# Kernel tuning notes

Measured on AMD Instinct MI355X. Metric: run time of the kernel, lower is better.

The kernel has to match this reference:

```python
import jax, jax.numpy as jnp
import numpy as np

B, S, E, H, FF = 8, 1024, 1024, 16, 4096
DK = E // H
EPS = 1.1920929e-07  # torch RMSNorm default eps = finfo(float32).eps


def _rmsnorm(x, g):
    return x * jax.lax.rsqrt(jnp.mean(x * x, axis=-1, keepdims=True) + EPS) * g


def _rope(q, k):
    # q, k: [B, H, S, DK]; standard rotate-half RoPE, theta=10000
    d = q.shape[-1]
    s = q.shape[-2]
    inv_freq = 1.0 / (10000.0 ** (jnp.arange(0, d, 2, dtype=jnp.float32) / d))
    ang = jnp.arange(s, dtype=jnp.float32)[:, None] * inv_freq  # [S, d/2]
    cos = jnp.concatenate([jnp.cos(ang), jnp.cos(ang)], axis=-1)  # [S, d]
    sin = jnp.concatenate([jnp.sin(ang), jnp.sin(ang)], axis=-1)

    def rot(x):
        x1, x2 = jnp.split(x, 2, axis=-1)
        return jnp.concatenate([-x2, x1], axis=-1)

    return q * cos + rot(q) * sin, k * cos + rot(k) * sin


def setup_inputs() -> dict:
    key = jax.random.key(0)
    ks = jax.random.split(key, 16)
    sc = 0.02
    inp = {
        "x": jax.random.normal(ks[0], (B, S, E), dtype=jnp.float32),
        "WQ": jax.random.normal(ks[1], (E, E), dtype=jnp.float32) * sc,
        "bQ": jnp.zeros((E,), jnp.float32),
        "WK": jax.random.normal(ks[2], (E, E), dtype=jnp.float32) * sc,
        "bK": jnp.zeros((E,), jnp.float32),
        "WV": jax.random.normal(ks[3], (E, E), dtype=jnp.float32) * sc,
        "bV": jnp.zeros((E,), jnp.float32),
        "WO": jax.random.normal(ks[4], (E, E), dtype=jnp.float32) * sc,
        "bO": jnp.zeros((E,), jnp.float32),
        "W1": jax.random.normal(ks[5], (E, FF), dtype=jnp.float32) * sc,
        "b1": jnp.zeros((FF,), jnp.float32),
        "W2": jax.random.normal(ks[6], (FF, E), dtype=jnp.float32) * sc,
        "b2": jnp.zeros((E,), jnp.float32),
        "g1": jnp.ones((E,), jnp.float32),
        "g2": jnp.ones((E,), jnp.float32),
    }
    return inp


def reference(x, WQ, bQ, WK, bK, WV, bV, WO, bO, W1, b1, W2, b2, g1, g2):
    b, s, e = x.shape

    def attn(h):
        q = (h @ WQ + bQ).reshape(b, s, H, DK).transpose(0, 2, 1, 3)
        k = (h @ WK + bK).reshape(b, s, H, DK).transpose(0, 2, 1, 3)
        v = (h @ WV + bV).reshape(b, s, H, DK).transpose(0, 2, 1, 3)
        q, k = _rope(q, k)
        scores = jnp.einsum("bhqd,bhkd->bhqk", q, k) / jnp.sqrt(jnp.float32(DK))
        p = jax.nn.softmax(scores, axis=-1)
        o = jnp.einsum("bhqk,bhkd->bhqd", p, v)
        o = o.transpose(0, 2, 1, 3).reshape(b, s, e)
        return o @ WO + bO

    def ffn(h):
        return jax.nn.relu(h @ W1 + b1) @ W2 + b2

    x = x + attn(_rmsnorm(x, g1))
    x = x + ffn(_rmsnorm(x, g2))
    return x
```

## Files before the change

kernel.cpp:

```cpp
#include <hip/hip_runtime.h>
#include <math.h>

#define B_ 8
#define S_ 1024
#define E_ 1024
#define H_ 16
#define FF_ 4096

typedef __attribute__((ext_vector_type(8))) short bf16x8;
typedef __attribute__((ext_vector_type(4))) float f32x4;

#define QSCALE 0.1803368801111f
#define LG2_10K 0.4152410118f

__device__ __forceinline__ unsigned short f2bf(float f) {
  union { float f; unsigned u; } v;
  v.f = f;
  unsigned r = v.u + 0x7fffu + ((v.u >> 16) & 1u);
  return (unsigned short)(r >> 16);
}
__device__ __forceinline__ float bf2f(unsigned short u) {
  union { unsigned u; float f; } v;
  v.u = ((unsigned)u) << 16;
  return v.f;
}
__device__ __forceinline__ unsigned fbits(float f) {
  union { float f; unsigned u; } v;
  v.f = f;
  return v.u;
}

__device__ __forceinline__ void glds16(const void* g, void* l) {
  __builtin_amdgcn_global_load_lds(
      (const __attribute__((address_space(1))) unsigned int*)g,
      (__attribute__((address_space(3))) unsigned int*)l, 16, 0, 0);
}

__global__ __launch_bounds__(256) void prep(const float* __restrict__ WQ,
                                            const float* __restrict__ WK,
                                            const float* __restrict__ WV,
                                            const float* __restrict__ WO,
                                            const float* __restrict__ W1,
                                            const float* __restrict__ W2,
                                            const float* __restrict__ bQ,
                                            const float* __restrict__ bK,
                                            const float* __restrict__ bV,
                                            unsigned short* __restrict__ WQKVt,
                                            unsigned short* __restrict__ WOt,
                                            unsigned short* __restrict__ W1t,
                                            unsigned short* __restrict__ W2t,
                                            float* __restrict__ bqkv) {
  const int id = blockIdx.x;
  if (id >= 12288) {
    const int i = (id - 12288) * 256 + threadIdx.x;
    if (i < 3072)
      bqkv[i] = (i < 1024) ? bQ[i] : ((i < 2048) ? bK[i - 1024] : bV[i - 2048]);
    return;
  }
  const float* W;
  unsigned short* D;
  int K, N, x, y;
  if (id < 4096) {
    const int m = id >> 10;
    const float* ws4[4] = {WQ, WK, WV, WO};
    unsigned short* ds4[4] = {WQKVt, WQKVt + 1024 * 1024, WQKVt + 2 * 1024 * 1024, WOt};
    W = ws4[m]; D = ds4[m]; K = 1024; N = 1024;
    x = id & 31; y = (id >> 5) & 31;
  } else if (id < 8192) {
    const int j = id - 4096;
    W = W1; D = W1t; K = 1024; N = 4096;
    x = j & 127; y = j >> 7;
  } else {
    const int j = id - 8192;
    W = W2; D = W2t; K = 4096; N = 1024;
    x = j & 31; y = j >> 5;
  }
  __shared__ float t[32][33];
  const int tx = threadIdx.x & 31, ty = threadIdx.x >> 5;
  const int n0 = x * 32, k0 = y * 32;
#pragma unroll
  for (int p = 0; p < 4; ++p)
    t[ty + p * 8][tx] = W[(size_t)(k0 + ty + p * 8) * N + n0 + tx];
  __syncthreads();
#pragma unroll
  for (int p = 0; p < 4; ++p)
    D[(size_t)(n0 + ty + p * 8) * K + k0 + tx] = f2bf(t[tx][ty + p * 8]);
}

__global__ __launch_bounds__(256) void rmsnorm_kernel(const float* __restrict__ x,
                                                      const float* __restrict__ g,
                                                      unsigned short* __restrict__ out) {
  const int row = blockIdx.x;
  const int t = threadIdx.x;
  const float4 v = ((const float4*)(x + (size_t)row * E_))[t];
  float ss = v.x * v.x + v.y * v.y + v.z * v.z + v.w * v.w;
#pragma unroll
  for (int off = 32; off > 0; off >>= 1) ss += __shfl_down(ss, off);
  __shared__ float sred[4];
  if ((t & 63) == 0) sred[t >> 6] = ss;
  __syncthreads();
  const float tot = sred[0] + sred[1] + sred[2] + sred[3];
  const float rinv = rsqrtf(tot * (1.0f / E_) + 1.1920929e-07f);
  const float4 gv = ((const float4*)g)[t];
  ushort4 o;
  o.x = f2bf(v.x * rinv * gv.x);
  o.y = f2bf(v.y * rinv * gv.y);
  o.z = f2bf(v.z * rinv * gv.z);
  o.w = f2bf(v.w * rinv * gv.w);
  ((ushort4*)(out + (size_t)row * E_))[t] = o;
}

template <int EPI, int SPLIT>
__global__ __launch_bounds__(512, 2) void gemm256(const unsigned short* __restrict__ A,
                                                  const unsigned short* __restrict__ Bt,
                                                  const float* __restrict__ bias,
                                                  unsigned short* __restrict__ C,
                                                  int M, int N, int K) {
  __shared__ unsigned short Ls[2][2][256 * 64];
  const int tid = threadIdx.x;
  const int w = tid >> 6;
  const int lane = tid & 63;

  int id = blockIdx.x;
  int kh = 0;
  int nb = gridDim.x;
  if (SPLIT) { kh = id >> 7; id &= 127; nb = 128; }
  const int lid = (id & 7) * (nb >> 3) + (id >> 3);
  const int nbn = N >> 8;
  const int bm = (lid / nbn) * 256;
  const int bn = (lid % nbn) * 256;

  const int Kloc = SPLIT ? (K >> 1) : K;
  const unsigned short* Ab = A + (size_t)kh * Kloc;
  const unsigned short* Bb = Bt + (size_t)kh * Kloc;

  const int wm = (w & 1) * 128, wn = (w >> 1) * 64;

  f32x4 acc[8][4];
#pragma unroll
  for (int i = 0; i < 8; ++i)
#pragma unroll
    for (int j = 0; j < 4; ++j) acc[i][j] = (f32x4){0.f, 0.f, 0.f, 0.f};

  const int srow = lane >> 3;
  const int skb = (lane & 7) ^ srow;
  const unsigned short* Ap[4];
  const unsigned short* Bp[4];
#pragma unroll
  for (int p = 0; p < 4; ++p) {
    const int u = w * 4 + p;
    Ap[p] = Ab + (size_t)(bm + u * 8 + srow) * K + skb * 8;
    Bp[p] = Bb + (size_t)(bn + u * 8 + srow) * K + skb * 8;
  }

  const int fr = lane & 15;
  const int g = lane >> 4;
  const int sw = fr & 7;

  bf16x8 av[4], bv[4];

#define STG2(tt, sb, p0, p1)                                                  \
  {                                                                           \
    glds16(Ap[p0] + (size_t)(tt) * 64, &Ls[sb][0][(w * 4 + p0) * 512 + lane * 8]); \
    glds16(Bp[p0] + (size_t)(tt) * 64, &Ls[sb][1][(w * 4 + p0) * 512 + lane * 8]); \
    glds16(Ap[p1] + (size_t)(tt) * 64, &Ls[sb][0][(w * 4 + p1) * 512 + lane * 8]); \
    glds16(Bp[p1] + (size_t)(tt) * 64, &Ls[sb][1][(w * 4 + p1) * 512 + lane * 8]); \
  }
#define RDA(cb, kc, h)                                                        \
  _Pragma("unroll") for (int i4 = 0; i4 < 4; ++i4)                            \
      av[i4] = *(const bf16x8*)&Ls[cb][0][(wm + ((h) * 4 + i4) * 16 + fr) * 64 + \
                                          (((kc) * 4 + g) ^ sw) * 8];
#define RDB(cb, kc)                                                           \
  _Pragma("unroll") for (int in = 0; in < 4; ++in)                            \
      bv[in] = *(const bf16x8*)&Ls[cb][1][(wn + in * 16 + fr) * 64 +          \
                                          (((kc) * 4 + g) ^ sw) * 8];
#define LWAIT asm volatile("s_waitcnt lgkmcnt(0)" ::: "memory");
#define VDRAIN asm volatile("s_waitcnt vmcnt(0)" ::: "memory");
#define MFMA16(h)                                                             \
  __builtin_amdgcn_s_setprio(1);                                              \
  _Pragma("unroll") for (int i4 = 0; i4 < 4; ++i4)                            \
  _Pragma("unroll") for (int in = 0; in < 4; ++in)                            \
      acc[(h) * 4 + i4][in] = __builtin_amdgcn_mfma_f32_16x16x32_bf16(        \
          av[i4], bv[in], acc[(h) * 4 + i4][in], 0, 0, 0);                    \
  __builtin_amdgcn_s_setprio(0);

  const int nt = Kloc >> 6;
  const int ni = nt >> 1;

  STG2(0, 0, 0, 1);
  STG2(0, 0, 2, 3);
  VDRAIN;
  __builtin_amdgcn_s_barrier();

  for (int i = 0; i < ni; ++i) {
    const int t1 = 2 * i + 1;
    const int t2 = 2 * i + 2;

    RDB(0, 0); RDA(0, 0, 0);
    STG2(t1, 1, 0, 1);
    __builtin_amdgcn_s_barrier();
    LWAIT; MFMA16(0);
    __builtin_amdgcn_s_barrier();
    RDA(0, 0, 1);
    STG2(t1, 1, 2, 3);
    __builtin_amdgcn_s_barrier();
    LWAIT; MFMA16(1);
    __builtin_amdgcn_s_barrier();
    RDB(0, 1); RDA(0, 1, 0);
    __builtin_amdgcn_s_barrier();
    LWAIT; MFMA16(0);
    __builtin_amdgcn_s_barrier();
    RDA(0, 1, 1);
    __builtin_amdgcn_s_barrier();
    LWAIT; MFMA16(1);
    VDRAIN;
    __builtin_amdgcn_s_barrier();
    RDB(1, 0); RDA(1, 0, 0);
    if (t2 < nt) STG2(t2, 0, 0, 1);
    __builtin_amdgcn_s_barrier();
    LWAIT; MFMA16(0);
    __builtin_amdgcn_s_barrier();
    RDA(1, 0, 1);
    if (t2 < nt) STG2(t2, 0, 2, 3);
    __builtin_amdgcn_s_barrier();
    LWAIT; MFMA16(1);
    __builtin_amdgcn_s_barrier();
    RDB(1, 1); RDA(1, 1, 0);
    __builtin_amdgcn_s_barrier();
    LWAIT; MFMA16(0);
    __builtin_amdgcn_s_barrier();
    RDA(1, 1, 1);
    __builtin_amdgcn_s_barrier();
    LWAIT; MFMA16(1);
    VDRAIN;
    __builtin_amdgcn_s_barrier();
  }

  if (EPI == 0) {
#pragma unroll
    for (int im = 0; im < 8; ++im) {
      const int row0 = bm + wm + im * 16 + g * 4;
#pragma unroll
      for (int in = 0; in < 4; ++in) {
        const int col = bn + wn + in * 16 + fr;
        const float bvv = bias[col];
#pragma unroll
        for (int r = 0; r < 4; ++r) {
          float v = acc[im][in][r] + bvv;
          v = fmaxf(v, 0.0f);
          C[(size_t)(row0 + r) * N + col] = f2bf(v);
        }
      }
    }
  } else {
    unsigned short* P = C + (size_t)kh * ((size_t)M * N);
#pragma unroll
    for (int im = 0; im < 8; ++im) {
      const int row0 = bm + wm + im * 16 + g * 4;
#pragma unroll
      for (int in = 0; in < 4; ++in) {
        const int col = bn + wn + in * 16 + fr;
#pragma unroll
        for (int r = 0; r < 4; ++r)
          P[(size_t)(row0 + r) * N + col] = f2bf(acc[im][in][r]);
      }
    }
  }
#undef STG2
#undef RDA
#undef RDB
#undef LWAIT
#undef VDRAIN
#undef MFMA16
}

__global__ __launch_bounds__(256) void ff2_reduce(const unsigned short* __restrict__ Pp,
                                                  const float* __restrict__ x1,
                                                  const float* __restrict__ b2,
                                                  float* __restrict__ out) {
  const int i = blockIdx.x * 256 + threadIdx.x;
  const size_t off = (size_t)i * 4;
  const ushort4 p0 = *(const ushort4*)(Pp + off);
  const ushort4 p1 = *(const ushort4*)(Pp + (8u << 20) + off);
  const float4 xv = *(const float4*)(x1 + off);
  const float4 bv = *(const float4*)(b2 + (off & 1023));
  float4 o;
  o.x = xv.x + bv.x + bf2f(p0.x) + bf2f(p1.x);
  o.y = xv.y + bv.y + bf2f(p0.y) + bf2f(p1.y);
  o.z = xv.z + bv.z + bf2f(p0.z) + bf2f(p1.z);
  o.w = xv.w + bv.w + bf2f(p0.w) + bf2f(p1.w);
  *(float4*)(out + off) = o;
}

template <int OUT_BF16, int RELU, int RES>
__global__ __launch_bounds__(256) void gemm_n64(const unsigned short* __restrict__ A,
                                                const unsigned short* __restrict__ Bt,
                                                const float* __restrict__ bias,
                                                const float* __restrict__ res,
                                                void* __restrict__ C,
                                                int M, int N, int K) {
  __shared__ unsigned short As[128 * 64];
  __shared__ unsigned short Bs[64 * 64];
  const int tid = threadIdx.x;
  const int w = tid >> 6;
  const int lane = tid & 63;

  const int nbn = N >> 6;
  const int bm = (blockIdx.x / nbn) * 128;
  const int bn = (blockIdx.x % nbn) * 64;

  const int wm = (w & 1) * 64, wn = (w >> 1) * 32;

  f32x4 acc[4][2];
#pragma unroll
  for (int i = 0; i < 4; ++i)
#pragma unroll
    for (int j = 0; j < 2; ++j) acc[i][j] = (f32x4){0.f, 0.f, 0.f, 0.f};

  const int srow = lane >> 3;
  const int skb = (lane & 7) ^ srow;
  const unsigned short* Ap[4];
  const unsigned short* Bp[2];
  unsigned short* AsD[4];
  unsigned short* BsD[2];
#pragma unroll
  for (int p = 0; p < 4; ++p) {
    const int u = w * 4 + p;
    Ap[p] = A + (size_t)(bm + u * 8 + srow) * K + skb * 8;
    AsD[p] = &As[u * 512 + lane * 8];
  }
#pragma unroll
  for (int p = 0; p < 2; ++p) {
    const int u = w * 2 + p;
    Bp[p] = Bt + (size_t)(bn + u * 8 + srow) * K + skb * 8;
    BsD[p] = &Bs[u * 512 + lane * 8];
  }

  const int fr = lane & 15;
  const int g = lane >> 4;
  const int sw = fr & 7;

  for (int k0 = 0; k0 < K; k0 += 64) {
    __syncthreads();
#pragma unroll
    for (int p = 0; p < 4; ++p) glds16(Ap[p] + k0, AsD[p]);
#pragma unroll
    for (int p = 0; p < 2; ++p) glds16(Bp[p] + k0, BsD[p]);
    __syncthreads();
    bf16x8 a[4][2], b[2][2];
#pragma unroll
    for (int im = 0; im < 4; ++im)
#pragma unroll
      for (int kc = 0; kc < 2; ++kc)
        a[im][kc] = *(const bf16x8*)&As[(wm + im * 16 + fr) * 64 + ((kc * 4 + g) ^ sw) * 8];
#pragma unroll
    for (int in = 0; in < 2; ++in)
#pragma unroll
      for (int kc = 0; kc < 2; ++kc)
        b[in][kc] = *(const bf16x8*)&Bs[(wn + in * 16 + fr) * 64 + ((kc * 4 + g) ^ sw) * 8];
#pragma unroll
    for (int im = 0; im < 4; ++im)
#pragma unroll
      for (int in = 0; in < 2; ++in) {
        acc[im][in] = __builtin_amdgcn_mfma_f32_16x16x32_bf16(a[im][0], b[in][0], acc[im][in], 0, 0, 0);
        acc[im][in] = __builtin_amdgcn_mfma_f32_16x16x32_bf16(a[im][1], b[in][1], acc[im][in], 0, 0, 0);
      }
  }

#pragma unroll
  for (int im = 0; im < 4; ++im) {
    const int row0 = bm + wm + im * 16 + (lane >> 4) * 4;
#pragma unroll
    for (int in = 0; in < 2; ++in) {
      const int col = bn + wn + in * 16 + fr;
      const float bv = bias[col];
#pragma unroll
      for (int r = 0; r < 4; ++r) {
        float v = acc[im][in][r] + bv;
        if (RES) v += res[(size_t)(row0 + r) * N + col];
        if (RELU) v = fmaxf(v, 0.0f);
        if (OUT_BF16)
          ((unsigned short*)C)[(size_t)(row0 + r) * N + col] = f2bf(v);
        else
          ((float*)C)[(size_t)(row0 + r) * N + col] = v;
      }
    }
  }
}

__global__ __launch_bounds__(256) void gemm_qkv(const unsigned short* __restrict__ A,
                                                const unsigned short* __restrict__ Bt,
                                                const float* __restrict__ bias,
                                                unsigned short* __restrict__ QKV,
                                                unsigned short* __restrict__ Vt,
                                                int M, int K) {
  __shared__ unsigned short As[128 * 64];
  __shared__ unsigned short Bs[128 * 64];
  const int tid = threadIdx.x;
  const int w = tid >> 6;
  const int lane = tid & 63;

  const int nb = gridDim.x;
  const int id = blockIdx.x;
  const int lid = (id & 7) * (nb >> 3) + (id >> 3);
  const int per = (M >> 7) * 8;
  const int grp = lid / per;
  const int rem = lid - grp * per;
  const int bn = (grp * 8 + (rem & 7)) * 128;
  const int bm = (rem >> 3) * 128;

  const int wm = (w & 1) * 64, wn = (w >> 1) * 64;

  f32x4 acc[4][4];
#pragma unroll
  for (int i = 0; i < 4; ++i)
#pragma unroll
    for (int j = 0; j < 4; ++j) acc[i][j] = (f32x4){0.f, 0.f, 0.f, 0.f};

  const int srow = lane >> 3;
  const int skb = (lane & 7) ^ srow;
  const unsigned short* Ap[4];
  const unsigned short* Bp[4];
  unsigned short* AsD[4];
  unsigned short* BsD[4];
#pragma unroll
  for (int p = 0; p < 4; ++p) {
    const int u = w * 4 + p;
    Ap[p] = A + (size_t)(bm + u * 8 + srow) * K + skb * 8;
    Bp[p] = Bt + (size_t)(bn + u * 8 + srow) * K + skb * 8;
    AsD[p] = &As[u * 512 + lane * 8];
    BsD[p] = &Bs[u * 512 + lane * 8];
  }

  const int fr = lane & 15;
  const int g = lane >> 4;
  const int sw = fr & 7;

  for (int k0 = 0; k0 < K; k0 += 64) {
    __syncthreads();
#pragma unroll
    for (int p = 0; p < 4; ++p) glds16(Ap[p] + k0, AsD[p]);
#pragma unroll
    for (int p = 0; p < 4; ++p) glds16(Bp[p] + k0, BsD[p]);
    __syncthreads();
    bf16x8 a[4][2], b[4][2];
#pragma unroll
    for (int im = 0; im < 4; ++im)
#pragma unroll
      for (int kc = 0; kc < 2; ++kc)
        a[im][kc] = *(const bf16x8*)&As[(wm + im * 16 + fr) * 64 + ((kc * 4 + g) ^ sw) * 8];
#pragma unroll
    for (int in = 0; in < 4; ++in)
#pragma unroll
      for (int kc = 0; kc < 2; ++kc)
        b[in][kc] = *(const bf16x8*)&Bs[(wn + in * 16 + fr) * 64 + ((kc * 4 + g) ^ sw) * 8];
#pragma unroll
    for (int im = 0; im < 4; ++im)
#pragma unroll
      for (int in = 0; in < 4; ++in) {
        acc[im][in] = __builtin_amdgcn_mfma_f32_16x16x32_bf16(a[im][0], b[in][0], acc[im][in], 0, 0, 0);
        acc[im][in] = __builtin_amdgcn_mfma_f32_16x16x32_bf16(a[im][1], b[in][1], acc[im][in], 0, 0, 0);
      }
  }

  const int cbase = bn + wn;
  const int seg = cbase >> 6;
  const int typ = seg >> 4;
  const int hh = seg & 15;
  const int bidx = bm >> 10;
  float bv[4];
#pragma unroll
  for (int in = 0; in < 4; ++in) bv[in] = bias[cbase + in * 16 + fr];

  if (typ == 2) {
#pragma unroll
    for (int im = 0; im < 4; ++im) {
      const int s0 = (bm & 1023) + wm + im * 16 + (lane >> 4) * 4;
#pragma unroll
      for (int in = 0; in < 4; ++in) {
        const int d = in * 16 + fr;
        ushort4 o4;
        o4.x = f2bf(acc[im][in][0] + bv[in]);
        o4.y = f2bf(acc[im][in][1] + bv[in]);
        o4.z = f2bf(acc[im][in][2] + bv[in]);
        o4.w = f2bf(acc[im][in][3] + bv[in]);
        *(ushort4*)&Vt[(size_t)((bidx * 16 + hh) * 64 + d) * S_ + s0] = o4;
      }
    }
  } else {
    const float qs = (typ == 0) ? QSCALE : 1.0f;
    const float i0 = exp2f(-LG2_10K * (float)fr);
    const float i1 = exp2f(-LG2_10K * (float)(fr + 16));
#pragma unroll
    for (int im = 0; im < 4; ++im) {
      const int row0 = bm + wm + im * 16 + (lane >> 4) * 4;
#pragma unroll
      for (int r = 0; r < 4; ++r) {
        const int row = row0 + r;
        const float s = (float)(row & 1023);
        float sn0, cs0, sn1, cs1;
        __sincosf(s * i0, &sn0, &cs0);
        __sincosf(s * i1, &sn1, &cs1);
        const float x0 = acc[im][0][r] + bv[0];
        const float x1 = acc[im][1][r] + bv[1];
        const float x2 = acc[im][2][r] + bv[2];
        const float x3 = acc[im][3][r] + bv[3];
        unsigned short* cp = QKV + (size_t)row * 3072 + cbase;
        cp[fr]      = f2bf((x0 * cs0 - x2 * sn0) * qs);
        cp[16 + fr] = f2bf((x1 * cs1 - x3 * sn1) * qs);
        cp[32 + fr] = f2bf((x2 * cs0 + x0 * sn0) * qs);
        cp[48 + fr] = f2bf((x3 * cs1 + x1 * sn1) * qs);
      }
    }
  }
}

__global__ __launch_bounds__(256) void attn_v4(const unsigned short* __restrict__ QKV,
                                               const unsigned short* __restrict__ Vt,
                                               unsigned short* __restrict__ Og) {
  __shared__ unsigned short Kf[2][8 * 512];
  __shared__ unsigned short Vf[2][8 * 512];
  __shared__ unsigned short Ps[4][32 * 72];
  const int tid = threadIdx.x;
  const int w = tid >> 6, lane = tid & 63;
  const int qt = blockIdx.x, bh = blockIdx.y;
  const int b = bh >> 4, h = bh & 15;
  const int fr = lane & 15, g = lane >> 4, fk = g * 8;
  const int q0w = qt * 128 + w * 32;

  bf16x8 qB[2][2];
#pragma unroll
  for (int nt = 0; nt < 2; ++nt)
#pragma unroll
    for (int c = 0; c < 2; ++c)
      qB[nt][c] = *(const bf16x8*)&QKV[(size_t)(b * S_ + q0w + nt * 16 + fr) * 3072 +
                                       h * 64 + c * 32 + fk];

  f32x4 o[4][2];
#pragma unroll
  for (int mt = 0; mt < 4; ++mt)
#pragma unroll
    for (int nt = 0; nt < 2; ++nt) o[mt][nt] = (f32x4){0.f, 0.f, 0.f, 0.f};
  float l[2] = {0.0f, 0.0f};

#define STAGE(kt, bufi)                                                                   \
  {                                                                                       \
    _Pragma("unroll") for (int p = 0; p < 4; ++p) {                                       \
      const int u = w * 4 + p;                                                            \
      if (u < 8) {                                                                        \
        const int mt = u >> 1, c = u & 1;                                                 \
        glds16(QKV + (size_t)(b * S_ + (kt) * 64 + mt * 16 + fr) * 3072 + 1024 + h * 64 + \
                   c * 32 + fk,                                                           \
               &Kf[bufi][u * 512]);                                                       \
      } else {                                                                            \
        const int v2 = u - 8, mt = v2 >> 1, c = v2 & 1;                                   \
        glds16(Vt + (size_t)(bh * 64 + mt * 16 + fr) * S_ + (kt) * 64 + c * 32 + fk,      \
               &Vf[bufi][v2 * 512]);                                                      \
      }                                                                                   \
    }                                                                                     \
  }

  STAGE(0, 0);

  for (int kt = 0; kt < 16; ++kt) {
    __syncthreads();
    if (kt < 15) STAGE(kt + 1, (kt + 1) & 1);
    const unsigned short* Kc = Kf[kt & 1];
    const unsigned short* Vc = Vf[kt & 1];

    f32x4 s[4][2];
#pragma unroll
    for (int mt = 0; mt < 4; ++mt) {
      const bf16x8 k0 = *(const bf16x8*)&Kc[(mt * 2 + 0) * 512 + lane * 8];
      const bf16x8 k1 = *(const bf16x8*)&Kc[(mt * 2 + 1) * 512 + lane * 8];
#pragma unroll
      for (int nt = 0; nt < 2; ++nt) {
        f32x4 a = (f32x4){0.f, 0.f, 0.f, 0.f};
        a = __builtin_amdgcn_mfma_f32_16x16x32_bf16(k0, qB[nt][0], a, 0, 0, 0);
        a = __builtin_amdgcn_mfma_f32_16x16x32_bf16(k1, qB[nt][1], a, 0, 0, 0);
        s[mt][nt] = a;
      }
    }

#pragma unroll
    for (int nt = 0; nt < 2; ++nt) {
      float rs = 0.0f;
#pragma unroll
      for (int mt = 0; mt < 4; ++mt)
#pragma unroll
        for (int r = 0; r < 4; ++r) {
          const float p = exp2f(s[mt][nt][r]);
          s[mt][nt][r] = p;
          rs += p;
        }
      rs += __shfl_xor(rs, 16);
      rs += __shfl_xor(rs, 32);
      l[nt] += rs;
    }

#pragma unroll
    for (int nt = 0; nt < 2; ++nt)
#pragma unroll
      for (int mt = 0; mt < 4; ++mt) {
        uint2 pk;
        pk.x = __builtin_amdgcn_perm(fbits(s[mt][nt][1]), fbits(s[mt][nt][0]), 0x07060302u);
        pk.y = __builtin_amdgcn_perm(fbits(s[mt][nt][3]), fbits(s[mt][nt][2]), 0x07060302u);
        *(uint2*)&Ps[w][(nt * 16 + fr) * 72 + mt * 16 + g * 4] = pk;
      }

    bf16x8 pB[2][2];
#pragma unroll
    for (int nt = 0; nt < 2; ++nt)
#pragma unroll
      for (int c = 0; c < 2; ++c)
        pB[nt][c] = *(const bf16x8*)&Ps[w][(nt * 16 + fr) * 72 + c * 32 + fk];
#pragma unroll
    for (int mt = 0; mt < 4; ++mt) {
      const bf16x8 v0 = *(const bf16x8*)&Vc[(mt * 2 + 0) * 512 + lane * 8];
      const bf16x8 v1 = *(const bf16x8*)&Vc[(mt * 2 + 1) * 512 + lane * 8];
#pragma unroll
      for (int nt = 0; nt < 2; ++nt) {
        o[mt][nt] = __builtin_amdgcn_mfma_f32_16x16x32_bf16(v0, pB[nt][0], o[mt][nt], 0, 0, 0);
        o[mt][nt] = __builtin_amdgcn_mfma_f32_16x16x32_bf16(v1, pB[nt][1], o[mt][nt], 0, 0, 0);
      }
    }
  }

  const float linv0 = 1.0f / l[0], linv1 = 1.0f / l[1];
#pragma unroll
  for (int nt = 0; nt < 2; ++nt) {
    const float li = nt ? linv1 : linv0;
#pragma unroll
    for (int mt = 0; mt < 4; ++mt) {
      uint2 pk;
      pk.x = __builtin_amdgcn_perm(fbits(o[mt][nt][1] * li), fbits(o[mt][nt][0] * li), 0x07060302u);
      pk.y = __builtin_amdgcn_perm(fbits(o[mt][nt][3] * li), fbits(o[mt][nt][2] * li), 0x07060302u);
      *(uint2*)&Ps[w][(nt * 16 + fr) * 72 + mt * 16 + g * 4] = pk;
    }
  }
  const int qr = lane >> 1, hf = lane & 1;
#pragma unroll
  for (int c = 0; c < 2; ++c) {
    const bf16x8 vv = *(const bf16x8*)&Ps[w][qr * 72 + hf * 16 + c * 32];
    *(bf16x8*)&Og[(size_t)(b * S_ + q0w + qr) * E_ + h * 64 + hf * 16 + c * 32] = vv;
  }
}

extern "C" void kernel_launch(void* const* d_in, const int* in_sizes, int n_in,
                              void* d_out, int out_size, void* d_ws, size_t ws_size,
                              hipStream_t stream) {
  const float* x  = (const float*)d_in[0];
  const float* WQ = (const float*)d_in[1];
  const float* bQ = (const float*)d_in[2];
  const float* WK = (const float*)d_in[3];
  const float* bK = (const float*)d_in[4];
  const float* WV = (const float*)d_in[5];
  const float* bV = (const float*)d_in[6];
  const float* WO = (const float*)d_in[7];
  const float* bO = (const float*)d_in[8];
  const float* W1 = (const float*)d_in[9];
  const float* b1 = (const float*)d_in[10];
  const float* W2 = (const float*)d_in[11];
  const float* b2 = (const float*)d_in[12];
  const float* g1 = (const float*)d_in[13];
  const float* g2 = (const float*)d_in[14];
  float* out = (float*)d_out;

  char* ws = (char*)d_ws;
  const size_t MB = 1024 * 1024;
  unsigned short* h1   = (unsigned short*)(ws + 0 * MB);
  unsigned short* QKV  = (unsigned short*)(ws + 16 * MB);
  unsigned short* Vt   = (unsigned short*)(ws + 64 * MB);
  unsigned short* Ob   = (unsigned short*)(ws + 80 * MB);
  float*          x1   = (float*)(ws + 96 * MB);
  unsigned short* h2   = (unsigned short*)(ws + 128 * MB);
  unsigned short* mid  = (unsigned short*)(ws + 16 * MB);
  unsigned short* WQKVt= (unsigned short*)(ws + 144 * MB);
  unsigned short* WOt  = (unsigned short*)(ws + 150 * MB);
  unsigned short* W1t  = (unsigned short*)(ws + 152 * MB);
  unsigned short* W2t  = (unsigned short*)(ws + 160 * MB);
  float*          bqkv = (float*)(ws + 168 * MB);
  unsigned short* Pp   = (unsigned short*)(ws + 176 * MB);

  const int M = B_ * S_;

  prep<<<12300, 256, 0, stream>>>(WQ, WK, WV, WO, W1, W2, bQ, bK, bV,
                                  WQKVt, WOt, W1t, W2t, bqkv);

  rmsnorm_kernel<<<M, 256, 0, stream>>>(x, g1, h1);

  gemm_qkv<<<24 * 64, 256, 0, stream>>>(h1, WQKVt, bqkv, QKV, Vt, M, E_);

  attn_v4<<<dim3(8, B_ * H_), 256, 0, stream>>>(QKV, Vt, Ob);

  gemm_n64<0, 0, 1><<<64 * 16, 256, 0, stream>>>(Ob, WOt, bO, x, x1, M, E_, E_);

  rmsnorm_kernel<<<M, 256, 0, stream>>>(x1, g2, h2);

  gemm256<0, 0><<<512, 512, 0, stream>>>(h2, W1t, b1, mid, M, FF_, E_);

  gemm256<1, 1><<<256, 512, 0, stream>>>(mid, W2t, nullptr, Pp, M, 1024, 4096);

  ff2_reduce<<<8192, 256, 0, stream>>>(Pp, x1, b2, out);
}
```

Before: 505.5 us.

## Rework GEMM pipelines: double-buffered prefetch loop, dedicated FF2 kernel, wider out-proj tile

The generic 256x256 GEMM main loop becomes a simpler double-buffered pipeline. Two k-tiles are prefetched up front, with a partial vmcnt wait and one barrier pair per tile, replacing the many fine-grained barriers. The old interleaved schedule moves into a dedicated FF2 split-K kernel (gemm256p) with hardcoded shapes and grouped block swizzling. The output projection GEMM goes from 128x64 to 128x128 tiles with a grouped block ordering, raising per-block MFMA reuse but halving the grid and using more registers.

After: 467.4 us. 1.08x faster.

```diff
diff --git a/kernel.cpp b/kernel.cpp
--- a/kernel.cpp
+++ b/kernel.cpp
@@ -157,6 +157,130 @@
   const int g = lane >> 4;
   const int sw = fr & 7;
 
+#define ISSUE256(tt, bi)                                              \
+  {                                                                   \
+    _Pragma("unroll") for (int p = 0; p < 4; ++p) {                   \
+      const int u = w * 4 + p;                                        \
+      glds16(Ap[p] + (size_t)(tt) * 64, &Ls[bi][0][u * 512 + lane * 8]); \
+    }                                                                 \
+    _Pragma("unroll") for (int p = 0; p < 4; ++p) {                   \
+      const int u = w * 4 + p;                                        \
+      glds16(Bp[p] + (size_t)(tt) * 64, &Ls[bi][1][u * 512 + lane * 8]); \
+    }                                                                 \
+  }
+
+  const int nt = Kloc >> 6;
+  ISSUE256(0, 0);
+  ISSUE256(1, 1);
+
+  for (int t = 0; t < nt; ++t) {
+    if (t < nt - 1)
+      asm volatile("s_waitcnt vmcnt(8)" ::: "memory");
+    else
+      asm volatile("s_waitcnt vmcnt(0)" ::: "memory");
+    __builtin_amdgcn_s_barrier();
+    __builtin_amdgcn_sched_barrier(0);
+
+    const unsigned short* Ac = &Ls[t & 1][0][0];
+    const unsigned short* Bc = &Ls[t & 1][1][0];
+#pragma unroll
+    for (int kc = 0; kc < 2; ++kc) {
+      bf16x8 a[8], b[4];
+#pragma unroll
+      for (int im = 0; im < 8; ++im)
+        a[im] = *(const bf16x8*)&Ac[(wm + im * 16 + fr) * 64 + (((kc * 4 + g) ^ sw)) * 8];
+#pragma unroll
+      for (int in = 0; in < 4; ++in)
+        b[in] = *(const bf16x8*)&Bc[(wn + in * 16 + fr) * 64 + (((kc * 4 + g) ^ sw)) * 8];
+      __builtin_amdgcn_s_setprio(1);
+#pragma unroll
+      for (int im = 0; im < 8; ++im)
+#pragma unroll
+        for (int in = 0; in < 4; ++in)
+          acc[im][in] = __builtin_amdgcn_mfma_f32_16x16x32_bf16(a[im], b[in], acc[im][in], 0, 0, 0);
+      __builtin_amdgcn_s_setprio(0);
+    }
+
+    __builtin_amdgcn_sched_barrier(0);
+    __builtin_amdgcn_s_barrier();
+    if (t + 2 < nt) ISSUE256(t + 2, t & 1);
+  }
+
+  if (EPI == 0) {
+#pragma unroll
+    for (int im = 0; im < 8; ++im) {
+      const int row0 = bm + wm + im * 16 + g * 4;
+#pragma unroll
+      for (int in = 0; in < 4; ++in) {
+        const int col = bn + wn + in * 16 + fr;
+        const float bv = bias[col];
+#pragma unroll
+        for (int r = 0; r < 4; ++r) {
+          float v = acc[im][in][r] + bv;
+          v = fmaxf(v, 0.0f);
+          C[(size_t)(row0 + r) * N + col] = f2bf(v);
+        }
+      }
+    }
+  } else {
+    unsigned short* P = C + (size_t)kh * ((size_t)M * N);
+#pragma unroll
+    for (int im = 0; im < 8; ++im) {
+      const int row0 = bm + wm + im * 16 + g * 4;
+#pragma unroll
+      for (int in = 0; in < 4; ++in) {
+        const int col = bn + wn + in * 16 + fr;
+#pragma unroll
+        for (int r = 0; r < 4; ++r)
+          P[(size_t)(row0 + r) * N + col] = f2bf(acc[im][in][r]);
+      }
+    }
+  }
+#undef ISSUE256
+}
+
+__global__ __launch_bounds__(512, 1) void gemm256p(const unsigned short* __restrict__ A,
+                                                   const unsigned short* __restrict__ Bt,
+                                                   unsigned short* __restrict__ Pp) {
+  const int M = 8192, N = 1024, K = 4096, KH = 2048;
+  __shared__ unsigned short Ls[2][2][256 * 64];
+  const int tid = threadIdx.x;
+  const int w = tid >> 6;
+  const int lane = tid & 63;
+
+  int id = blockIdx.x;
+  const int kh = id >> 7;
+  id &= 127;
+  const int lid = (id & 7) * 16 + (id >> 3);
+  const int bm = (lid >> 2) * 256;
+  const int bn = (lid & 3) * 256;
+
+  const unsigned short* Ab = A + (size_t)kh * KH;
+  const unsigned short* Bb = Bt + (size_t)kh * KH;
+
+  const int wm = (w & 1) * 128, wn = (w >> 1) * 64;
+
+  f32x4 acc[8][4];
+#pragma unroll
+  for (int i = 0; i < 8; ++i)
+#pragma unroll
+    for (int j = 0; j < 4; ++j) acc[i][j] = (f32x4){0.f, 0.f, 0.f, 0.f};
+
+  const int srow = lane >> 3;
+  const int skb = (lane & 7) ^ srow;
+  const unsigned short* Ap[4];
+  const unsigned short* Bp[4];
+#pragma unroll
+  for (int p = 0; p < 4; ++p) {
+    const int u = w * 4 + p;
+    Ap[p] = Ab + (size_t)(bm + u * 8 + srow) * K + skb * 8;
+    Bp[p] = Bb + (size_t)(bn + u * 8 + srow) * K + skb * 8;
+  }
+
+  const int fr = lane & 15;
+  const int g = lane >> 4;
+  const int sw = fr & 7;
+
   bf16x8 av[4], bv[4];
 
 #define STG2(tt, sb, p0, p1)                                                  \
@@ -184,7 +308,7 @@
           av[i4], bv[in], acc[(h) * 4 + i4][in], 0, 0, 0);                    \
   __builtin_amdgcn_s_setprio(0);
 
-  const int nt = Kloc >> 6;
+  const int nt = KH >> 6;
   const int ni = nt >> 1;
 
   STG2(0, 0, 0, 1);
@@ -201,34 +325,41 @@
     __builtin_amdgcn_s_barrier();
     LWAIT; MFMA16(0);
     __builtin_amdgcn_s_barrier();
+
     RDA(0, 0, 1);
     STG2(t1, 1, 2, 3);
     __builtin_amdgcn_s_barrier();
     LWAIT; MFMA16(1);
     __builtin_amdgcn_s_barrier();
+
     RDB(0, 1); RDA(0, 1, 0);
     __builtin_amdgcn_s_barrier();
     LWAIT; MFMA16(0);
     __builtin_amdgcn_s_barrier();
+
     RDA(0, 1, 1);
     __builtin_amdgcn_s_barrier();
     LWAIT; MFMA16(1);
     VDRAIN;
     __builtin_amdgcn_s_barrier();
+
     RDB(1, 0); RDA(1, 0, 0);
     if (t2 < nt) STG2(t2, 0, 0, 1);
     __builtin_amdgcn_s_barrier();
     LWAIT; MFMA16(0);
     __builtin_amdgcn_s_barrier();
+
     RDA(1, 0, 1);
     if (t2 < nt) STG2(t2, 0, 2, 3);
     __builtin_amdgcn_s_barrier();
     LWAIT; MFMA16(1);
     __builtin_amdgcn_s_barrier();
+
     RDB(1, 1); RDA(1, 1, 0);
     __builtin_amdgcn_s_barrier();
     LWAIT; MFMA16(0);
     __builtin_amdgcn_s_barrier();
+
     RDA(1, 1, 1);
     __builtin_amdgcn_s_barrier();
     LWAIT; MFMA16(1);
@@ -236,34 +367,16 @@
     __builtin_amdgcn_s_barrier();
   }
 
-  if (EPI == 0) {
-#pragma unroll
-    for (int im = 0; im < 8; ++im) {
-      const int row0 = bm + wm + im * 16 + g * 4;
-#pragma unroll
-      for (int in = 0; in < 4; ++in) {
-        const int col = bn + wn + in * 16 + fr;
-        const float bvv = bias[col];
-#pragma unroll
-        for (int r = 0; r < 4; ++r) {
-          float v = acc[im][in][r] + bvv;
-          v = fmaxf(v, 0.0f);
-          C[(size_t)(row0 + r) * N + col] = f2bf(v);
-        }
-      }
-    }
-  } else {
-    unsigned short* P = C + (size_t)kh * ((size_t)M * N);
-#pragma unroll
-    for (int im = 0; im < 8; ++im) {
-      const int row0 = bm + wm + im * 16 + g * 4;
-#pragma unroll
-      for (int in = 0; in < 4; ++in) {
-        const int col = bn + wn + in * 16 + fr;
-#pragma unroll
-        for (int r = 0; r < 4; ++r)
-          P[(size_t)(row0 + r) * N + col] = f2bf(acc[im][in][r]);
-      }
+  unsigned short* P = Pp + (size_t)kh * ((size_t)M * N);
+#pragma unroll
+  for (int im = 0; im < 8; ++im) {
+    const int row0 = bm + wm + im * 16 + g * 4;
+#pragma unroll
+    for (int in = 0; in < 4; ++in) {
+      const int col = bn + wn + in * 16 + fr;
+#pragma unroll
+      for (int r = 0; r < 4; ++r)
+        P[(size_t)(row0 + r) * N + col] = f2bf(acc[im][in][r]);
     }
   }
 #undef STG2
@@ -293,46 +406,47 @@
 }
 
 template <int OUT_BF16, int RELU, int RES>
-__global__ __launch_bounds__(256) void gemm_n64(const unsigned short* __restrict__ A,
-                                                const unsigned short* __restrict__ Bt,
-                                                const float* __restrict__ bias,
-                                                const float* __restrict__ res,
-                                                void* __restrict__ C,
-                                                int M, int N, int K) {
+__global__ __launch_bounds__(256) void gemm_bf16(const unsigned short* __restrict__ A,
+                                                 const unsigned short* __restrict__ Bt,
+                                                 const float* __restrict__ bias,
+                                                 const float* __restrict__ res,
+                                                 void* __restrict__ C,
+                                                 int M, int N, int K) {
   __shared__ unsigned short As[128 * 64];
-  __shared__ unsigned short Bs[64 * 64];
+  __shared__ unsigned short Bs[128 * 64];
   const int tid = threadIdx.x;
   const int w = tid >> 6;
   const int lane = tid & 63;
 
-  const int nbn = N >> 6;
-  const int bm = (blockIdx.x / nbn) * 128;
-  const int bn = (blockIdx.x % nbn) * 64;
-
-  const int wm = (w & 1) * 64, wn = (w >> 1) * 32;
-
-  f32x4 acc[4][2];
+  const int nb = gridDim.x;
+  const int id = blockIdx.x;
+  const int lid = (id & 7) * (nb >> 3) + (id >> 3);
+  const int per = (M >> 7) * 8;
+  const int grp = lid / per;
+  const int rem = lid - grp * per;
+  const int bn = (grp * 8 + (rem & 7)) * 128;
+  const int bm = (rem >> 3) * 128;
+
+  const int wm = (w & 1) * 64, wn = (w >> 1) * 64;
+
+  f32x4 acc[4][4];
 #pragma unroll
   for (int i = 0; i < 4; ++i)
 #pragma unroll
-    for (int j = 0; j < 2; ++j) acc[i][j] = (f32x4){0.f, 0.f, 0.f, 0.f};
+    for (int j = 0; j < 4; ++j) acc[i][j] = (f32x4){0.f, 0.f, 0.f, 0.f};
 
   const int srow = lane >> 3;
   const int skb = (lane & 7) ^ srow;
   const unsigned short* Ap[4];
-  const unsigned short* Bp[2];
+  const unsigned short* Bp[4];
   unsigned short* AsD[4];
-  unsigned short* BsD[2];
+  unsigned short* BsD[4];
 #pragma unroll
   for (int p = 0; p < 4; ++p) {
     const int u = w * 4 + p;
     Ap[p] = A + (size_t)(bm + u * 8 + srow) * K + skb * 8;
+    Bp[p] = Bt + (size_t)(bn + u * 8 + srow) * K + skb * 8;
     AsD[p] = &As[u * 512 + lane * 8];
-  }
-#pragma unroll
-  for (int p = 0; p < 2; ++p) {
-    const int u = w * 2 + p;
-    Bp[p] = Bt + (size_t)(bn + u * 8 + srow) * K + skb * 8;
     BsD[p] = &Bs[u * 512 + lane * 8];
   }
 
@@ -345,23 +459,23 @@
 #pragma unroll
     for (int p = 0; p < 4; ++p) glds16(Ap[p] + k0, AsD[p]);
 #pragma unroll
-    for (int p = 0; p < 2; ++p) glds16(Bp[p] + k0, BsD[p]);
+    for (int p = 0; p < 4; ++p) glds16(Bp[p] + k0, BsD[p]);
     __syncthreads();
-    bf16x8 a[4][2], b[2][2];
+    bf16x8 a[4][2], b[4][2];
 #pragma unroll
     for (int im = 0; im < 4; ++im)
 #pragma unroll
       for (int kc = 0; kc < 2; ++kc)
         a[im][kc] = *(const bf16x8*)&As[(wm + im * 16 + fr) * 64 + ((kc * 4 + g) ^ sw) * 8];
 #pragma unroll
-    for (int in = 0; in < 2; ++in)
+    for (int in = 0; in < 4; ++in)
 #pragma unroll
       for (int kc = 0; kc < 2; ++kc)
         b[in][kc] = *(const bf16x8*)&Bs[(wn + in * 16 + fr) * 64 + ((kc * 4 + g) ^ sw) * 8];
 #pragma unroll
     for (int im = 0; im < 4; ++im)
 #pragma unroll
-      for (int in = 0; in < 2; ++in) {
+      for (int in = 0; in < 4; ++in) {
         acc[im][in] = __builtin_amdgcn_mfma_f32_16x16x32_bf16(a[im][0], b[in][0], acc[im][in], 0, 0, 0);
         acc[im][in] = __builtin_amdgcn_mfma_f32_16x16x32_bf16(a[im][1], b[in][1], acc[im][in], 0, 0, 0);
       }
@@ -371,7 +485,7 @@
   for (int im = 0; im < 4; ++im) {
     const int row0 = bm + wm + im * 16 + (lane >> 4) * 4;
 #pragma unroll
-    for (int in = 0; in < 2; ++in) {
+    for (int in = 0; in < 4; ++in) {
       const int col = bn + wn + in * 16 + fr;
       const float bv = bias[col];
 #pragma unroll
@@ -693,13 +807,13 @@
 
   attn_v4<<<dim3(8, B_ * H_), 256, 0, stream>>>(QKV, Vt, Ob);
 
-  gemm_n64<0, 0, 1><<<64 * 16, 256, 0, stream>>>(Ob, WOt, bO, x, x1, M, E_, E_);
+  gemm_bf16<0, 0, 1><<<64 * 8, 256, 0, stream>>>(Ob, WOt, bO, x, x1, M, E_, E_);
 
   rmsnorm_kernel<<<M, 256, 0, stream>>>(x1, g2, h2);
 
   gemm256<0, 0><<<512, 512, 0, stream>>>(h2, W1t, b1, mid, M, FF_, E_);
 
-  gemm256<1, 1><<<256, 512, 0, stream>>>(mid, W2t, nullptr, Pp, M, 1024, 4096);
+  gemm256p<<<256, 512, 0, stream>>>(mid, W2t, Pp);
 
   ff2_reduce<<<8192, 256, 0, stream>>>(Pp, x1, b2, out);
 }
```
